# Kernel optimization log

Hardware: AMD Instinct MI355X
Metric: run time of the kernel (lower is better)

Reference implementation:

```python
import jax, jax.numpy as jnp
import numpy as np
from math import sqrt

NOISE_STD = 0.05
ALPHA = 0.2
RHO = 1.0
B, T, I, H, O, R = 64, 2048, 3, 512, 1, 1


def setup_inputs() -> dict:
    key = jax.random.key(0)
    ks = jax.random.split(key, 8)
    return {
        'input': jax.random.normal(ks[0], (B, T, I), dtype=jnp.float32),
        'noise': jax.random.normal(ks[1], (B, T, H), dtype=jnp.float32),
        'w_i': jax.random.normal(ks[2], (I, H), dtype=jnp.float32),
        's_i': jnp.ones((I,), dtype=jnp.float32),
        'm_rec': jax.random.normal(ks[3], (H, R), dtype=jnp.float32),
        'n_rec': jax.random.normal(ks[4], (H, R), dtype=jnp.float32),
        'rec_noise': jax.random.normal(ks[5], (H, H), dtype=jnp.float32) * (RHO / sqrt(H)),
        'w_o': jax.random.normal(ks[6], (H, O), dtype=jnp.float32),
        's_o': jnp.ones((O,), dtype=jnp.float32),
        'h0': jnp.zeros((H,), dtype=jnp.float32),
    }


def reference(input, noise, w_i, s_i, m_rec, n_rec, rec_noise, w_o, s_o, h0):
    hidden = h0.shape[0]
    # proxy parameters (define_proxy_parameters)
    w_rec = m_rec @ n_rec.T / hidden + rec_noise          # [H, H]
    wi_full = w_i * s_i[:, None]                          # [I, H]
    wo_full = w_o * s_o                                   # [H, O]
    # per-step additive drive: noise_std*noise + alpha * (input @ wi_full)
    drive = NOISE_STD * noise + ALPHA * jnp.einsum('bti,ih->bth', input, wi_full)  # [B,T,H]
    h_init = jnp.broadcast_to(h0, (input.shape[0], hidden))

    def step(h, d_t):
        r = jnp.tanh(h)
        h_new = h + d_t + ALPHA * (-h + r @ w_rec.T)
        return h_new, jnp.tanh(h_new)

    _, r_seq = jax.lax.scan(step, h_init, jnp.swapaxes(drive, 0, 1))  # r_seq: [T,B,H]
    output = jnp.einsum('tbh,ho->bto', r_seq, wo_full) / hidden        # [B,T,O]
    return output
```

## Files before the change

kernel.cpp:

```cpp
#include <hip/hip_runtime.h>

constexpr int Bc = 64;
constexpr int Tc = 2048;
constexpr int Ic = 3;
constexpr int Hc = 512;
constexpr float AL = 0.2f;
constexpr float NS = 0.05f;
constexpr int NSL = 4;
constexpr int HS  = Hc / NSL;

__global__ void prep_wt(const float* __restrict__ m, const float* __restrict__ n,
                        const float* __restrict__ rn, float* __restrict__ WT, int R) {
    int id = blockIdx.x * 256 + threadIdx.x;
    if (id >= Hc * Hc) return;
    int k = id >> 9;
    int h = id & (Hc - 1);
    float acc = rn[h * Hc + k];
    for (int r = 0; r < R; ++r)
        acc = fmaf(m[h * R + r], n[k * R + r] * (1.0f / Hc), acc);
    WT[id] = acc;
}

__launch_bounds__(512, 1)
__global__ void rnn4(const float* __restrict__ input, const float* __restrict__ noise,
                     const float* __restrict__ w_i, const float* __restrict__ s_i,
                     const float* __restrict__ WT, const float* __restrict__ w_o,
                     const float* __restrict__ s_o, const float* __restrict__ h0,
                     float* __restrict__ out, unsigned long long* __restrict__ rbuf) {
    __shared__ float r_lds[Hc];
    __shared__ float pl[NSL][HS];
    __shared__ float red[8];

    const int tid = threadIdx.x;
    const int s   = blockIdx.x >> 6;
    const int b   = blockIdx.x & 63;
    const int g   = tid >> 7;
    const int j   = tid & 127;
    const int hbase = s * HS;

    float w[128];
    const float* Wp = WT + (size_t)(g * 128) * Hc + hbase + j;
    #pragma unroll
    for (int kk = 0; kk < 128; ++kk) w[kk] = Wp[(size_t)kk * Hc];

    const float wo_t = w_o[tid] * s_o[0] * (1.0f / Hc);

    float h = 0.f, wi0 = 0.f, wi1 = 0.f, wi2 = 0.f;
    if (tid < HS) {
        h   = h0[hbase + tid];
        wi0 = w_i[0 * Hc + hbase + tid] * s_i[0];
        wi1 = w_i[1 * Hc + hbase + tid] * s_i[1];
        wi2 = w_i[2 * Hc + hbase + tid] * s_i[2];
    }
    r_lds[tid] = tanhf(h0[tid]);

    const float* noise_b = noise + (size_t)b * Tc * Hc;
    const float* inp_b   = input + (size_t)b * Tc * Ic;
    unsigned long long* rb_b = rbuf + (size_t)b * 2 * Hc;

    float nz = (tid < HS) ? noise_b[hbase + tid] : 0.f;
    float i0 = inp_b[0], i1 = inp_b[1], i2 = inp_b[2];
    __syncthreads();

    for (int t = 0; t < Tc; ++t) {
        const int tn = (t + 1 < Tc) ? t + 1 : t;
        const float nz_n = (tid < HS) ? noise_b[(size_t)tn * Hc + hbase + tid] : 0.f;
        const float i0n = inp_b[tn * Ic + 0];
        const float i1n = inp_b[tn * Ic + 1];
        const float i2n = inp_b[tn * Ic + 2];

        const float* rg = r_lds + g * 128;
        float a0 = 0.f, a1 = 0.f, a2 = 0.f, a3 = 0.f;
        #pragma unroll
        for (int kk = 0; kk < 128; kk += 4) {
            const float4 rv = *(const float4*)(rg + kk);
            a0 = fmaf(w[kk + 0], rv.x, a0);
            a1 = fmaf(w[kk + 1], rv.y, a1);
            a2 = fmaf(w[kk + 2], rv.z, a2);
            a3 = fmaf(w[kk + 3], rv.w, a3);
        }
        pl[g][j] = (a0 + a1) + (a2 + a3);
        __syncthreads();

        const unsigned want = (unsigned)(t + 1);
        unsigned long long* slot = rb_b + ((size_t)((t + 1) & 1)) * Hc;

        if (tid < HS) {
            const float y  = pl[0][tid] + pl[1][tid] + pl[2][tid] + pl[3][tid];
            const float di = i0 * wi0 + i1 * wi1 + i2 * wi2;
            h = h + (NS * nz + AL * di) + AL * (y - h);
            const float rv = tanhf(h);
            r_lds[hbase + tid] = rv;
            const unsigned long long word =
                ((unsigned long long)want << 32) | (unsigned long long)__float_as_uint(rv);
            __hip_atomic_store(&slot[hbase + tid], word,
                               __ATOMIC_RELAXED, __HIP_MEMORY_SCOPE_AGENT);
        }

        if ((tid >> 7) != s) {
            const unsigned long long* myp = &slot[tid];
            unsigned long long v;
            for (;;) {
                v = __hip_atomic_load(myp, __ATOMIC_RELAXED, __HIP_MEMORY_SCOPE_AGENT);
                if ((unsigned)(v >> 32) == want) break;
                __builtin_amdgcn_s_sleep(1);
            }
            r_lds[tid] = __uint_as_float((unsigned)v);
        }
        __syncthreads();

        if ((t & 3) == s) {
            float p = r_lds[tid] * wo_t;
            #pragma unroll
            for (int off = 32; off; off >>= 1) p += __shfl_xor(p, off, 64);
            if ((tid & 63) == 0) red[tid >> 6] = p;
            __syncthreads();
            if (tid == 0)
                out[(size_t)b * Tc + t] = red[0] + red[1] + red[2] + red[3] +
                                          red[4] + red[5] + red[6] + red[7];
        }

        nz = nz_n; i0 = i0n; i1 = i1n; i2 = i2n;
    }
}

__launch_bounds__(512)
__global__ void rnn_scan_fb(const float* __restrict__ input, const float* __restrict__ noise,
                            const float* __restrict__ w_i, const float* __restrict__ s_i,
                            const float* __restrict__ WT, const float* __restrict__ w_o,
                            const float* __restrict__ s_o, const float* __restrict__ h0,
                            float* __restrict__ out) {
    __shared__ float r_lds[Hc];
    __shared__ float pl[4][Hc];
    __shared__ float wi_lds[Ic][Hc];
    __shared__ float red[8];

    const int tid = threadIdx.x;
    const int b   = blockIdx.x;
    const int g   = tid >> 7;
    const int j   = tid & 127;

    for (int i = 0; i < Ic; ++i) wi_lds[i][tid] = w_i[i * Hc + tid] * s_i[i];

    float h = h0[tid];
    float r_cur = tanhf(h);
    const float wo_h = w_o[tid] * s_o[0] * (1.0f / Hc);
    const float* noise_b = noise + (size_t)b * Tc * Hc;
    const float* inp_b   = input + (size_t)b * Tc * Ic;
    float nz = noise_b[tid];
    float i0 = inp_b[0], i1 = inp_b[1], i2 = inp_b[2];
    const float* Wg = WT + (g * 128) * Hc + 4 * j;
    const float* rg = r_lds + g * 128;
    __syncthreads();

    for (int t = 0; t < Tc; ++t) {
        const int tn = (t + 1 < Tc) ? t + 1 : t;
        const float nz_n = noise_b[(size_t)tn * Hc + tid];
        const float i0n = inp_b[tn * Ic + 0];
        const float i1n = inp_b[tn * Ic + 1];
        const float i2n = inp_b[tn * Ic + 2];

        r_lds[tid] = r_cur;
        __syncthreads();
        float a0 = 0.f, a1 = 0.f, a2 = 0.f, a3 = 0.f;
        #pragma unroll 4
        for (int kk = 0; kk < 128; kk += 4) {
            const float4 rv = *(const float4*)(rg + kk);
            const float4 w0 = *(const float4*)(Wg + (kk + 0) * Hc);
            const float4 w1 = *(const float4*)(Wg + (kk + 1) * Hc);
            const float4 w2 = *(const float4*)(Wg + (kk + 2) * Hc);
            const float4 w3 = *(const float4*)(Wg + (kk + 3) * Hc);
            a0 = fmaf(rv.x, w0.x, a0); a0 = fmaf(rv.y, w1.x, a0);
            a0 = fmaf(rv.z, w2.x, a0); a0 = fmaf(rv.w, w3.x, a0);
            a1 = fmaf(rv.x, w0.y, a1); a1 = fmaf(rv.y, w1.y, a1);
            a1 = fmaf(rv.z, w2.y, a1); a1 = fmaf(rv.w, w3.y, a1);
            a2 = fmaf(rv.x, w0.z, a2); a2 = fmaf(rv.y, w1.z, a2);
            a2 = fmaf(rv.z, w2.z, a2); a2 = fmaf(rv.w, w3.z, a2);
            a3 = fmaf(rv.x, w0.w, a3); a3 = fmaf(rv.y, w1.w, a3);
            a3 = fmaf(rv.z, w2.w, a3); a3 = fmaf(rv.w, w3.w, a3);
        }
        *(float4*)&pl[g][4 * j] = make_float4(a0, a1, a2, a3);
        __syncthreads();

        const float y  = pl[0][tid] + pl[1][tid] + pl[2][tid] + pl[3][tid];
        const float di = i0 * wi_lds[0][tid] + i1 * wi_lds[1][tid] + i2 * wi_lds[2][tid];
        h = h + (NS * nz + AL * di) + AL * (y - h);
        r_cur = tanhf(h);

        float p = r_cur * wo_h;
        #pragma unroll
        for (int off = 32; off; off >>= 1) p += __shfl_xor(p, off, 64);
        if ((tid & 63) == 0) red[tid >> 6] = p;
        __syncthreads();
        if (tid == 0)
            out[(size_t)b * Tc + t] = red[0] + red[1] + red[2] + red[3] +
                                      red[4] + red[5] + red[6] + red[7];
        nz = nz_n; i0 = i0n; i1 = i1n; i2 = i2n;
    }
}

extern "C" void kernel_launch(void* const* d_in, const int* in_sizes, int n_in,
                              void* d_out, int out_size, void* d_ws, size_t ws_size,
                              hipStream_t stream) {
    (void)n_in; (void)out_size;
    const float* input     = (const float*)d_in[0];
    const float* noise     = (const float*)d_in[1];
    const float* w_i       = (const float*)d_in[2];
    const float* s_i       = (const float*)d_in[3];
    const float* m_rec     = (const float*)d_in[4];
    const float* n_rec     = (const float*)d_in[5];
    const float* rec_noise = (const float*)d_in[6];
    const float* w_o       = (const float*)d_in[7];
    const float* s_o       = (const float*)d_in[8];
    const float* h0        = (const float*)d_in[9];
    float* out = (float*)d_out;

    const int R = in_sizes[4] / Hc;

    float* WT = (float*)d_ws;
    const size_t wt_bytes = (size_t)Hc * Hc * sizeof(float);
    const size_t rb_bytes = (size_t)Bc * 2 * Hc * sizeof(unsigned long long);

    prep_wt<<<(Hc * Hc + 255) / 256, 256, 0, stream>>>(m_rec, n_rec, rec_noise, WT, R);

    if (ws_size >= wt_bytes + rb_bytes) {
        unsigned long long* rbuf = (unsigned long long*)((char*)d_ws + wt_bytes);
        hipMemsetAsync(rbuf, 0, rb_bytes, stream);
        rnn4<<<NSL * Bc, 512, 0, stream>>>(input, noise, w_i, s_i, WT, w_o, s_o, h0,
                                           out, rbuf);
    } else {
        rnn_scan_fb<<<Bc, 512, 0, stream>>>(input, noise, w_i, s_i, WT, w_o, s_o, h0, out);
    }
}
```

Before: 3.875 ms.

## Reduce per-step partial sums with shuffles and double-buffer the LDS state

Each hidden unit is now handled by four adjacent lanes that split the K dimension. Their partial dot products are combined with wave shuffles, which removes the shared partial-sum array and one block barrier per timestep. The recurrent state is double-buffered in padded LDS. The spin on remote slices polls with sc0 global loads, no longer sleeps, and uses an atomic load only every fourth try. This adds tighter busy-polling, which raises memory traffic and risks relying on cache semantics of the sc0 load for cross-block visibility.

```diff
diff --git a/kernel.cpp b/kernel.cpp
--- a/kernel.cpp
+++ b/kernel.cpp
@@ -8,6 +8,7 @@
 constexpr float NS = 0.05f;
 constexpr int NSL = 4;
 constexpr int HS  = Hc / NSL;
+constexpr int PAD = 132;
 
 __global__ void prep_wt(const float* __restrict__ m, const float* __restrict__ n,
                         const float* __restrict__ rn, float* __restrict__ WT, int R) {
@@ -21,55 +22,65 @@
     WT[id] = acc;
 }
 
+__device__ __forceinline__ unsigned long long ld_sc0(const unsigned long long* p) {
+    unsigned long long v;
+    asm volatile("global_load_dwordx2 %0, %1, off sc0\n\t"
+                 "s_waitcnt vmcnt(0)"
+                 : "=v"(v) : "v"(p) : "memory");
+    return v;
+}
+
 __launch_bounds__(512, 1)
-__global__ void rnn4(const float* __restrict__ input, const float* __restrict__ noise,
-                     const float* __restrict__ w_i, const float* __restrict__ s_i,
-                     const float* __restrict__ WT, const float* __restrict__ w_o,
-                     const float* __restrict__ s_o, const float* __restrict__ h0,
-                     float* __restrict__ out, unsigned long long* __restrict__ rbuf) {
-    __shared__ float r_lds[Hc];
-    __shared__ float pl[NSL][HS];
+__global__ void rnn4r(const float* __restrict__ input, const float* __restrict__ noise,
+                      const float* __restrict__ w_i, const float* __restrict__ s_i,
+                      const float* __restrict__ WT, const float* __restrict__ w_o,
+                      const float* __restrict__ s_o, const float* __restrict__ h0,
+                      float* __restrict__ out, unsigned long long* __restrict__ rbuf) {
+    __shared__ float rp[2][NSL * PAD];
     __shared__ float red[8];
 
-    const int tid = threadIdx.x;
-    const int s   = blockIdx.x >> 6;
-    const int b   = blockIdx.x & 63;
-    const int g   = tid >> 7;
-    const int j   = tid & 127;
+    const int tid   = threadIdx.x;
+    const int s     = blockIdx.x >> 6;
+    const int b     = blockIdx.x & 63;
+    const int hl    = tid >> 2;
+    const int kg    = tid & 3;
     const int hbase = s * HS;
+    const int hmy   = hbase + hl;
 
     float w[128];
-    const float* Wp = WT + (size_t)(g * 128) * Hc + hbase + j;
+    const float* Wp = WT + (size_t)(kg * 128) * Hc + hmy;
     #pragma unroll
     for (int kk = 0; kk < 128; ++kk) w[kk] = Wp[(size_t)kk * Hc];
+    #pragma unroll
+    for (int kk = 0; kk < 128; ++kk) asm volatile("" : "+v"(w[kk]));
 
     const float wo_t = w_o[tid] * s_o[0] * (1.0f / Hc);
-
-    float h = 0.f, wi0 = 0.f, wi1 = 0.f, wi2 = 0.f;
-    if (tid < HS) {
-        h   = h0[hbase + tid];
-        wi0 = w_i[0 * Hc + hbase + tid] * s_i[0];
-        wi1 = w_i[1 * Hc + hbase + tid] * s_i[1];
-        wi2 = w_i[2 * Hc + hbase + tid] * s_i[2];
-    }
-    r_lds[tid] = tanhf(h0[tid]);
+    float h = h0[hmy];
+    const float wi0 = w_i[0 * Hc + hmy] * s_i[0];
+    const float wi1 = w_i[1 * Hc + hmy] * s_i[1];
+    const float wi2 = w_i[2 * Hc + hmy] * s_i[2];
+
+    rp[0][(tid >> 7) * PAD + (tid & 127)] = tanhf(h0[tid]);
 
     const float* noise_b = noise + (size_t)b * Tc * Hc;
     const float* inp_b   = input + (size_t)b * Tc * Ic;
     unsigned long long* rb_b = rbuf + (size_t)b * 2 * Hc;
 
-    float nz = (tid < HS) ? noise_b[hbase + tid] : 0.f;
+    float nz = noise_b[hmy];
     float i0 = inp_b[0], i1 = inp_b[1], i2 = inp_b[2];
+
+    const int ft   = tid + ((tid >= hbase) ? 128 : 0);
+    const int fpos = (ft >> 7) * PAD + (ft & 127);
     __syncthreads();
 
     for (int t = 0; t < Tc; ++t) {
         const int tn = (t + 1 < Tc) ? t + 1 : t;
-        const float nz_n = (tid < HS) ? noise_b[(size_t)tn * Hc + hbase + tid] : 0.f;
+        const float nz_n = noise_b[(size_t)tn * Hc + hmy];
         const float i0n = inp_b[tn * Ic + 0];
         const float i1n = inp_b[tn * Ic + 1];
         const float i2n = inp_b[tn * Ic + 2];
 
-        const float* rg = r_lds + g * 128;
+        const float* rg = &rp[t & 1][kg * PAD];
         float a0 = 0.f, a1 = 0.f, a2 = 0.f, a3 = 0.f;
         #pragma unroll
         for (int kk = 0; kk < 128; kk += 4) {
@@ -79,41 +90,47 @@
             a2 = fmaf(w[kk + 2], rv.z, a2);
             a3 = fmaf(w[kk + 3], rv.w, a3);
         }
-        pl[g][j] = (a0 + a1) + (a2 + a3);
-        __syncthreads();
+        float y = (a0 + a1) + (a2 + a3);
+        y += __shfl_xor(y, 1, 64);
+        y += __shfl_xor(y, 2, 64);
+
+        const float di = i0 * wi0 + i1 * wi1 + i2 * wi2;
+        h = h + (NS * nz + AL * di) + AL * (y - h);
+        const float rv_ = tanhf(h);
 
         const unsigned want = (unsigned)(t + 1);
         unsigned long long* slot = rb_b + ((size_t)((t + 1) & 1)) * Hc;
-
-        if (tid < HS) {
-            const float y  = pl[0][tid] + pl[1][tid] + pl[2][tid] + pl[3][tid];
-            const float di = i0 * wi0 + i1 * wi1 + i2 * wi2;
-            h = h + (NS * nz + AL * di) + AL * (y - h);
-            const float rv = tanhf(h);
-            r_lds[hbase + tid] = rv;
-            const unsigned long long word =
-                ((unsigned long long)want << 32) | (unsigned long long)__float_as_uint(rv);
-            __hip_atomic_store(&slot[hbase + tid], word,
+        float* wp_ = &rp[(t + 1) & 1][0];
+
+        if (kg == 0) {
+            __hip_atomic_store(&slot[hmy],
+                               ((unsigned long long)want << 32) |
+                               (unsigned long long)__float_as_uint(rv_),
                                __ATOMIC_RELAXED, __HIP_MEMORY_SCOPE_AGENT);
-        }
-
-        if ((tid >> 7) != s) {
-            const unsigned long long* myp = &slot[tid];
+            wp_[s * PAD + hl] = rv_;
+        }
+
+        if (tid < 384) {
+            const unsigned long long* p = &slot[ft];
             unsigned long long v;
+            int it = 0;
             for (;;) {
-                v = __hip_atomic_load(myp, __ATOMIC_RELAXED, __HIP_MEMORY_SCOPE_AGENT);
+                if ((it & 3) != 3)
+                    v = ld_sc0(p);
+                else
+                    v = __hip_atomic_load(p, __ATOMIC_RELAXED, __HIP_MEMORY_SCOPE_AGENT);
                 if ((unsigned)(v >> 32) == want) break;
-                __builtin_amdgcn_s_sleep(1);
+                ++it;
             }
-            r_lds[tid] = __uint_as_float((unsigned)v);
+            wp_[fpos] = __uint_as_float((unsigned)v);
         }
         __syncthreads();
 
         if ((t & 3) == s) {
-            float p = r_lds[tid] * wo_t;
+            float p2 = wp_[(tid >> 7) * PAD + (tid & 127)] * wo_t;
             #pragma unroll
-            for (int off = 32; off; off >>= 1) p += __shfl_xor(p, off, 64);
-            if ((tid & 63) == 0) red[tid >> 6] = p;
+            for (int off = 32; off; off >>= 1) p2 += __shfl_xor(p2, off, 64);
+            if ((tid & 63) == 0) red[tid >> 6] = p2;
             __syncthreads();
             if (tid == 0)
                 out[(size_t)b * Tc + t] = red[0] + red[1] + red[2] + red[3] +
@@ -226,8 +243,8 @@
     if (ws_size >= wt_bytes + rb_bytes) {
         unsigned long long* rbuf = (unsigned long long*)((char*)d_ws + wt_bytes);
         hipMemsetAsync(rbuf, 0, rb_bytes, stream);
-        rnn4<<<NSL * Bc, 512, 0, stream>>>(input, noise, w_i, s_i, WT, w_o, s_o, h0,
-                                           out, rbuf);
+        rnn4r<<<NSL * Bc, 512, 0, stream>>>(input, noise, w_i, s_i, WT, w_o, s_o, h0,
+                                            out, rbuf);
     } else {
         rnn_scan_fb<<<Bc, 512, 0, stream>>>(input, noise, w_i, s_i, WT, w_o, s_o, h0, out);
     }
```

After: 3.802 ms. No clear change (-1.9%).
